# Kernel optimization log

Measured on AMD Instinct MI355X. Metric: run time of the kernel, lower is better.

## Reference

```python
import jax, jax.numpy as jnp
import numpy as np

B, N, C = 8, 4096, 512
H, DK, DV = 8, 64, 64


def _xnorm(x, gamma):
    # L2 norm over last dim, keepdim; scale by per-head gamma
    nrm = jnp.sqrt(jnp.sum(x * x, axis=-1, keepdims=True))
    return x * gamma / nrm


def setup_inputs() -> dict:
    key = jax.random.key(0)
    ks = jax.random.split(key, 9)
    inp = {
        "queries": jax.random.normal(ks[0], (B, N, C), dtype=jnp.float32),
        "keys": jax.random.normal(ks[1], (B, N, C), dtype=jnp.float32),
        "values": jax.random.normal(ks[2], (B, N, C), dtype=jnp.float32),
        # Linear weights stored torch-style [out, in]; init.normal_(std=0.001), bias=0
        "Wq": jax.random.normal(ks[3], (H * DK, C), dtype=jnp.float32) * 0.001,
        "bq": jnp.zeros((H * DK,), dtype=jnp.float32),
        "Wk": jax.random.normal(ks[4], (H * DK, C), dtype=jnp.float32) * 0.001,
        "bk": jnp.zeros((H * DK,), dtype=jnp.float32),
        "Wv": jax.random.normal(ks[5], (H * DV, C), dtype=jnp.float32) * 0.001,
        "bv": jnp.zeros((H * DV,), dtype=jnp.float32),
        "Wo": jax.random.normal(ks[6], (C, H * DV), dtype=jnp.float32) * 0.001,
        "bo": jnp.zeros((C,), dtype=jnp.float32),
        "gamma": jax.random.normal(ks[7], (1, H, 1, 1), dtype=jnp.float32),
    }
    return inp


def reference(queries, keys, values, Wq, bq, Wk, bk, Wv, bv, Wo, bo, gamma):
    bs, nq, _ = queries.shape
    nk = keys.shape[1]
    # projections -> [b, h, n, d]
    q = (queries @ Wq.T + bq).reshape(bs, nq, H, DK).transpose(0, 2, 1, 3)
    k = (keys @ Wk.T + bk).reshape(bs, nk, H, DK).transpose(0, 2, 1, 3)
    v = (values @ Wv.T + bv).reshape(bs, nk, H, DV).transpose(0, 2, 1, 3)
    # kv: [b, h, dk, dv]  (small intermediate)
    kv = jnp.einsum('bhnk,bhnv->bhkv', k, v)
    kv_n = _xnorm(kv, gamma)     # norm over dv
    q_n = _xnorm(q, gamma)       # norm over dk
    out = jnp.einsum('bhnk,bhkv->bhnv', q_n, kv_n)  # [b,h,nq,dv]
    out = out.transpose(0, 2, 1, 3).reshape(bs, nq, H * DV)
    return out @ Wo.T + bo
```

## Files before the change

kernel.cpp:

```cpp
#include <hip/hip_runtime.h>


typedef __attribute__((ext_vector_type(4))) float f32x4;
typedef __attribute__((ext_vector_type(8))) short s16x8;
typedef __attribute__((ext_vector_type(4))) unsigned short u16x4;
typedef __attribute__((ext_vector_type(8))) unsigned short u16x8;
typedef __attribute__((ext_vector_type(2))) unsigned u32x2;

#define DEVFN __device__ __forceinline__

DEVFN unsigned short f2b(float f) {
  union { float f; unsigned u; } un; un.f = f;
  unsigned r = un.u + 0x7fffu + ((un.u >> 16) & 1u);
  return (unsigned short)(r >> 16);
}
DEVFN float b2f(unsigned short us) {
  union { unsigned u; float f; } un; un.u = ((unsigned)us) << 16;
  return un.f;
}
DEVFN unsigned pk2(float x0, float x1) {
  union { float f; unsigned u; } a, b;
  a.f = x0; b.f = x1;
  return __builtin_amdgcn_perm(b.u + 0x8000u, a.u + 0x8000u, 0x07060302u);
}
DEVFN void gl_lds16(const void* g, void* l) {
  __builtin_amdgcn_global_load_lds(
      (const __attribute__((address_space(1))) unsigned*)g,
      (__attribute__((address_space(3))) unsigned*)l, 16, 0, 0);
}

template <bool AF32, typename CT>
DEVFN void gemmN512(const void* Ain, const unsigned short* Bt,
                    const float* bias, CT* C, bool qnorm,
                    const float* gamma, int bx) {
  __shared__ __align__(16) char LA[4][8192];
  __shared__ __align__(16) char LB[4][32768];
  const int tid = threadIdx.x, lane = tid & 63, wid = tid >> 6;
  const int r = lane & 15, g = lane >> 4;
  const int mw = wid >> 3;
  const int nw = wid & 7;

  const char* BsS = (const char*)Bt + (long)(wid * 32 + (lane >> 2)) * 1024 +
                    (((lane & 3) ^ ((lane >> 3) & 3)) * 16);

  const char* AfS = nullptr;
  const char* AsS = nullptr;
  int awr = 0;
  if constexpr (AF32) {
    AfS = (const char*)Ain + (long)(bx * 128 + (tid >> 3)) * 2048 +
          (tid & 7) * 16;
    const int row = tid >> 3, p = tid & 7;
    awr = row * 64 + (((p >> 1) ^ ((row >> 1) & 3)) << 4) + (p & 1) * 8;
  } else {
    AsS = (const char*)Ain + (long)(bx * 128 + wid * 16 + (lane >> 2)) * 1024 +
          (((lane & 3) ^ ((lane >> 3) & 3)) * 16);
  }

  f32x4 acc[4][4] = {};
  f32x4 paA, paB;

#define SGB(BUF, KT)                                                           \
  gl_lds16(BsS + (KT)*64, LB[BUF] + wid * 2048);                               \
  gl_lds16(BsS + 16384 + (KT)*64, LB[BUF] + wid * 2048 + 1024);
#define SGA(BUF, KT)                                                           \
  if (wid < 8) { gl_lds16(AsS + (KT)*64, LA[BUF] + wid * 1024); }
#define LDA(P, KT) P = *reinterpret_cast<const f32x4*>(AfS + (KT)*128);
#define WRA(P, BUF)                                                            \
  {                                                                            \
    u32x2 w;                                                                   \
    w[0] = pk2(P[0], P[1]);                                                    \
    w[1] = pk2(P[2], P[3]);                                                    \
    *reinterpret_cast<u32x2*>(LA[BUF] + awr) = w;                              \
  }
#define COMPUTE(BUF)                                                           \
  {                                                                            \
    s16x8 a[4], b[4];                                                          \
    _Pragma("unroll") for (int i = 0; i < 4; ++i) {                            \
      int ar = mw * 64 + i * 16 + r;                                           \
      a[i] = *reinterpret_cast<const s16x8*>(                                  \
          LA[BUF] + ar * 64 + ((g ^ ((ar >> 1) & 3)) << 4));                   \
    }                                                                          \
    _Pragma("unroll") for (int j = 0; j < 4; ++j) {                            \
      int br = nw * 64 + j * 16 + r;                                           \
      b[j] = *reinterpret_cast<const s16x8*>(                                  \
          LB[BUF] + br * 64 + ((g ^ ((br >> 1) & 3)) << 4));                   \
    }                                                                          \
    _Pragma("unroll") for (int i = 0; i < 4; ++i)                              \
        _Pragma("unroll") for (int j = 0; j < 4; ++j) acc[i][j] =              \
        __builtin_amdgcn_mfma_f32_16x16x32_bf16(a[i], b[j], acc[i][j], 0, 0,   \
                                                0);                            \
  }

  if constexpr (AF32) {
    LDA(paA, 0) WRA(paA, 0)
    LDA(paB, 1) WRA(paB, 1)
  } else {
    SGA(0, 0) SGA(1, 1)
  }
  SGB(0, 0) SGB(1, 1)
  __syncthreads();

#pragma unroll 1
  for (int t0 = 0; t0 < 14; t0 += 2) {
    const int b2 = (t0 + 2) & 3, b3 = (t0 + 3) & 3;
    if constexpr (AF32) {
      LDA(paA, t0 + 2) LDA(paB, t0 + 3)
    }
    SGB(b2, t0 + 2) SGB(b3, t0 + 3)
    if constexpr (!AF32) { SGA(b2, t0 + 2) SGA(b3, t0 + 3) }
    COMPUTE(t0 & 3)
    COMPUTE((t0 + 1) & 3)
    if constexpr (AF32) { WRA(paA, b2) WRA(paB, b3) }
    __syncthreads();
  }
  COMPUTE(2)
  COMPUTE(3)

#undef SGB
#undef SGA
#undef LDA
#undef WRA
#undef COMPUTE

  const int crow0 = bx * 128 + mw * 64 + g * 4;
  const int ccol0 = nw * 64 + r;
#pragma unroll
  for (int j = 0; j < 4; ++j) {
    float bv = bias[ccol0 + j * 16];
#pragma unroll
    for (int i = 0; i < 4; ++i)
#pragma unroll
      for (int ii = 0; ii < 4; ++ii) acc[i][j][ii] += bv;
  }
  if (qnorm) {
    const float gam = gamma[nw];
#pragma unroll
    for (int i = 0; i < 4; ++i)
#pragma unroll
      for (int ii = 0; ii < 4; ++ii) {
        float s = 0.f;
#pragma unroll
        for (int j = 0; j < 4; ++j) s += acc[i][j][ii] * acc[i][j][ii];
        s += __shfl_xor(s, 1);
        s += __shfl_xor(s, 2);
        s += __shfl_xor(s, 4);
        s += __shfl_xor(s, 8);
        float sc = gam / sqrtf(s);
#pragma unroll
        for (int j = 0; j < 4; ++j) acc[i][j][ii] *= sc;
      }
  }
#pragma unroll
  for (int i = 0; i < 4; ++i)
#pragma unroll
    for (int j = 0; j < 4; ++j)
#pragma unroll
      for (int ii = 0; ii < 4; ++ii) {
        long row = crow0 + i * 16 + ii;
        int col = ccol0 + j * 16;
        if constexpr (sizeof(CT) == 2)
          C[row * 512 + col] = f2b(acc[i][j][ii]);
        else
          C[row * 512 + col] = acc[i][j][ii];
      }
}

__global__ __launch_bounds__(1024, 4)
void proj_qkv(const float* __restrict__ Aq, const float* __restrict__ Ak,
              const float* __restrict__ Av, const unsigned short* __restrict__ Bq,
              const unsigned short* __restrict__ Bk, const unsigned short* __restrict__ Bv,
              const float* __restrict__ bq, const float* __restrict__ bk,
              const float* __restrict__ bv, unsigned short* __restrict__ Cq,
              unsigned short* __restrict__ Ck, unsigned short* __restrict__ Cv,
              const float* __restrict__ gamma) {
  const int z = blockIdx.y;
  const float* A = z == 0 ? Aq : (z == 1 ? Ak : Av);
  const unsigned short* B = z == 0 ? Bq : (z == 1 ? Bk : Bv);
  const float* bias = z == 0 ? bq : (z == 1 ? bk : bv);
  unsigned short* C = z == 0 ? Cq : (z == 1 ? Ck : Cv);
  gemmN512<true, unsigned short>(A, B, bias, C, z == 0, gamma, blockIdx.x);
}

__global__ __launch_bounds__(1024, 4)
void gemm_final(const unsigned short* __restrict__ q, const unsigned short* __restrict__ Mt,
                const float* __restrict__ bo, float* __restrict__ out) {
  const int zb = blockIdx.y;
  gemmN512<false, float>(q + (long)zb * 2097152, Mt + (long)zb * 262144, bo,
                         out + (long)zb * 2097152, false, nullptr, blockIdx.x);
}

#define NCHUNK 8
__global__ __launch_bounds__(256, 2)
void kv_partial(const unsigned short* __restrict__ kq,
                const unsigned short* __restrict__ vq,
                float* __restrict__ part) {
  const int tid = threadIdx.x;
  const int chunk = blockIdx.x;
  const int bh = blockIdx.y;
  const int b = bh >> 3, h = bh & 7;
  __shared__ float ks[32][64];
  __shared__ float vs[32][64];
  const int dk0 = (tid & 15) * 4;
  const int dv0 = (tid >> 4) * 4;
  float acc[4][4] = {};
  const long nbase = (long)b * 4096 + chunk * 512;
  const int lrow = tid >> 3, lc8 = tid & 7;

  for (int sub = 0; sub < 16; ++sub) {
    long n0 = nbase + sub * 32;
    {
      long gofs = (n0 + lrow) * 512 + h * 64 + lc8 * 8;
      u16x8 kk = *reinterpret_cast<const u16x8*>(kq + gofs);
      u16x8 vv = *reinterpret_cast<const u16x8*>(vq + gofs);
      f32x4 k0 = {b2f(kk[0]), b2f(kk[1]), b2f(kk[2]), b2f(kk[3])};
      f32x4 k1 = {b2f(kk[4]), b2f(kk[5]), b2f(kk[6]), b2f(kk[7])};
      f32x4 v0 = {b2f(vv[0]), b2f(vv[1]), b2f(vv[2]), b2f(vv[3])};
      f32x4 v1 = {b2f(vv[4]), b2f(vv[5]), b2f(vv[6]), b2f(vv[7])};
      *reinterpret_cast<f32x4*>(&ks[lrow][lc8 * 8]) = k0;
      *reinterpret_cast<f32x4*>(&ks[lrow][lc8 * 8 + 4]) = k1;
      *reinterpret_cast<f32x4*>(&vs[lrow][lc8 * 8]) = v0;
      *reinterpret_cast<f32x4*>(&vs[lrow][lc8 * 8 + 4]) = v1;
    }
    __syncthreads();
#pragma unroll 4
    for (int n = 0; n < 32; ++n) {
      f32x4 kk = *reinterpret_cast<const f32x4*>(&ks[n][dk0]);
      f32x4 vv = *reinterpret_cast<const f32x4*>(&vs[n][dv0]);
#pragma unroll
      for (int a = 0; a < 4; ++a)
#pragma unroll
        for (int c = 0; c < 4; ++c)
          acc[a][c] += kk[a] * vv[c];
    }
    __syncthreads();
  }
  float* pg = part + ((long)chunk * 64 + bh) * 4096;
#pragma unroll
  for (int a = 0; a < 4; ++a) {
    f32x4 o = {acc[a][0], acc[a][1], acc[a][2], acc[a][3]};
    *reinterpret_cast<f32x4*>(pg + (dk0 + a) * 64 + dv0) = o;
  }
}

__global__ __launch_bounds__(256)
void kv_norm_mt(const float* __restrict__ part, const float* __restrict__ gamma,
                const unsigned short* __restrict__ Wo_b,
                unsigned short* __restrict__ Mt) {
  const int bh = blockIdx.x, h = bh & 7, b = bh >> 3;
  const int tid = threadIdx.x;
  __shared__ float kvs[4096];
  __shared__ float scale_s[64];
  __shared__ __align__(16) unsigned short kvn_l[64 * 72];

#pragma unroll
  for (int i = 0; i < 4; ++i) {
    int e4 = i * 256 + tid;
    const float* p = part + (long)bh * 4096 + e4 * 4;
    f32x4 s = {0.f, 0.f, 0.f, 0.f};
#pragma unroll
    for (int c = 0; c < NCHUNK; ++c) {
      f32x4 v = *reinterpret_cast<const f32x4*>(p + (long)c * 64 * 4096);
      s += v;
    }
    *reinterpret_cast<f32x4*>(kvs + e4 * 4) = s;
  }
  __syncthreads();
  if (tid < 64) {
    float s = 0.f;
    for (int dv = 0; dv < 64; ++dv) { float x = kvs[tid * 64 + dv]; s += x * x; }
    scale_s[tid] = gamma[h] / sqrtf(s);
  }
  __syncthreads();
#pragma unroll
  for (int i = 0; i < 4; ++i) {
    int e4 = i * 256 + tid;
    int row = e4 >> 4, c0 = (e4 & 15) * 4;
    float sc = scale_s[row];
    f32x4 v = *reinterpret_cast<const f32x4*>(kvs + e4 * 4);
    u16x4 o = {f2b(v[0] * sc), f2b(v[1] * sc), f2b(v[2] * sc), f2b(v[3] * sc)};
    *reinterpret_cast<u16x4*>(kvn_l + row * 72 + c0) = o;
  }
  __syncthreads();

  const int seg = tid >> 6;
  const int lane = tid & 63;
  const int r = lane & 15, g = lane >> 4;
  f32x4 acc[8][4] = {};
  s16x8 bf[2][4];
#pragma unroll
  for (int ks = 0; ks < 2; ++ks)
#pragma unroll
    for (int j = 0; j < 4; ++j)
      bf[ks][j] = *reinterpret_cast<const s16x8*>(
          kvn_l + (j * 16 + r) * 72 + ks * 32 + g * 8);
#pragma unroll
  for (int ks = 0; ks < 2; ++ks)
#pragma unroll
    for (int i = 0; i < 8; ++i) {
      s16x8 af = *reinterpret_cast<const s16x8*>(
          Wo_b + (long)(seg * 128 + i * 16 + r) * 512 + h * 64 + ks * 32 + g * 8);
#pragma unroll
      for (int j = 0; j < 4; ++j)
        acc[i][j] = __builtin_amdgcn_mfma_f32_16x16x32_bf16(af, bf[ks][j], acc[i][j], 0, 0, 0);
    }
#pragma unroll
  for (int i = 0; i < 8; ++i)
#pragma unroll
    for (int j = 0; j < 4; ++j)
#pragma unroll
      for (int ii = 0; ii < 4; ++ii) {
        int c = seg * 128 + i * 16 + g * 4 + ii;
        int dk = j * 16 + r;
        Mt[(long)b * 262144 + (long)c * 512 + h * 64 + dk] = f2b(acc[i][j][ii]);
      }
}

__global__ void cast4(const float* __restrict__ a0, const float* __restrict__ a1,
                      const float* __restrict__ a2, const float* __restrict__ a3,
                      unsigned short* __restrict__ o0, unsigned short* __restrict__ o1,
                      unsigned short* __restrict__ o2, unsigned short* __restrict__ o3) {
  const int y = blockIdx.y;
  const float* in = y == 0 ? a0 : (y == 1 ? a1 : (y == 2 ? a2 : a3));
  unsigned short* out = y == 0 ? o0 : (y == 1 ? o1 : (y == 2 ? o2 : o3));
  int i = blockIdx.x * 256 + threadIdx.x;
  f32x4 v = reinterpret_cast<const f32x4*>(in)[i];
  reinterpret_cast<u16x4*>(out)[i] = u16x4{f2b(v[0]), f2b(v[1]), f2b(v[2]), f2b(v[3])};
}

extern "C" void kernel_launch(void* const* d_in, const int* in_sizes, int n_in,
                              void* d_out, int out_size, void* d_ws, size_t ws_size,
                              hipStream_t stream) {
  const float* queries = (const float*)d_in[0];
  const float* keys    = (const float*)d_in[1];
  const float* values  = (const float*)d_in[2];
  const float* Wq = (const float*)d_in[3];
  const float* bq = (const float*)d_in[4];
  const float* Wk = (const float*)d_in[5];
  const float* bk = (const float*)d_in[6];
  const float* Wv = (const float*)d_in[7];
  const float* bv = (const float*)d_in[8];
  const float* Wo = (const float*)d_in[9];
  const float* bo = (const float*)d_in[10];
  const float* gamma = (const float*)d_in[11];

  unsigned short* Wq_b = (unsigned short*)d_ws;
  unsigned short* Wk_b = Wq_b + 262144;
  unsigned short* Wv_b = Wk_b + 262144;
  unsigned short* Wo_b = Wv_b + 262144;
  unsigned short* q_b  = Wo_b + 262144;
  unsigned short* kvn  = q_b + 16777216;
  float* part = (float*)(kvn + 262144);
  unsigned short* Mt = (unsigned short*)(part + 2097152);
  unsigned short* k_b = (unsigned short*)d_out;
  unsigned short* v_b = k_b + 16777216;
  float* out = (float*)d_out;

  cast4<<<dim3(256, 4), 256, 0, stream>>>(Wq, Wk, Wv, Wo, Wq_b, Wk_b, Wv_b, Wo_b);

  proj_qkv<<<dim3(256, 3), 1024, 0, stream>>>(
      queries, keys, values, Wq_b, Wk_b, Wv_b, bq, bk, bv, q_b, k_b, v_b, gamma);

  kv_partial<<<dim3(NCHUNK, 64), 256, 0, stream>>>(k_b, v_b, part);
  kv_norm_mt<<<64, 256, 0, stream>>>(part, gamma, Wo_b, Mt);

  gemm_final<<<dim3(32, 8), 1024, 0, stream>>>(q_b, Mt, bo, out);
}
```

Before: 167.4 us.

## Restructure kv_partial so each wave owns a full 64x64 tile over row slices

The kv_partial kernel no longer stages K and V tiles through shared memory with per-subtile barriers. Each wave now reads bf16 K/V rows straight from global memory into registers and accumulates a full 64x64 outer-product tile over its own 128-row slice, with each lane holding an 8x8 block. The four wave partials are then reduced serially through shared memory before a coalesced store. This removes LDS traffic and barriers from the inner loop, but raises register pressure to 64 accumulators per lane, relies on global loads without LDS reuse, and adds a serialized cross-wave reduction.

```diff
diff --git a/kernel.cpp b/kernel.cpp
--- a/kernel.cpp
+++ b/kernel.cpp
@@ -194,51 +194,63 @@
 void kv_partial(const unsigned short* __restrict__ kq,
                 const unsigned short* __restrict__ vq,
                 float* __restrict__ part) {
-  const int tid = threadIdx.x;
+  const int tid = threadIdx.x, lane = tid & 63, wid = tid >> 6;
   const int chunk = blockIdx.x;
   const int bh = blockIdx.y;
   const int b = bh >> 3, h = bh & 7;
-  __shared__ float ks[32][64];
-  __shared__ float vs[32][64];
-  const int dk0 = (tid & 15) * 4;
-  const int dv0 = (tid >> 4) * 4;
-  float acc[4][4] = {};
-  const long nbase = (long)b * 4096 + chunk * 512;
-  const int lrow = tid >> 3, lc8 = tid & 7;
-
-  for (int sub = 0; sub < 16; ++sub) {
-    long n0 = nbase + sub * 32;
-    {
-      long gofs = (n0 + lrow) * 512 + h * 64 + lc8 * 8;
-      u16x8 kk = *reinterpret_cast<const u16x8*>(kq + gofs);
-      u16x8 vv = *reinterpret_cast<const u16x8*>(vq + gofs);
-      f32x4 k0 = {b2f(kk[0]), b2f(kk[1]), b2f(kk[2]), b2f(kk[3])};
-      f32x4 k1 = {b2f(kk[4]), b2f(kk[5]), b2f(kk[6]), b2f(kk[7])};
-      f32x4 v0 = {b2f(vv[0]), b2f(vv[1]), b2f(vv[2]), b2f(vv[3])};
-      f32x4 v1 = {b2f(vv[4]), b2f(vv[5]), b2f(vv[6]), b2f(vv[7])};
-      *reinterpret_cast<f32x4*>(&ks[lrow][lc8 * 8]) = k0;
-      *reinterpret_cast<f32x4*>(&ks[lrow][lc8 * 8 + 4]) = k1;
-      *reinterpret_cast<f32x4*>(&vs[lrow][lc8 * 8]) = v0;
-      *reinterpret_cast<f32x4*>(&vs[lrow][lc8 * 8 + 4]) = v1;
+  const int dk0 = (lane & 7) * 8;
+  const int dv0 = (lane >> 3) * 8;
+  __shared__ float red[4096];
+
+  f32x4 acc[8][2] = {};
+  const long nbase = (long)b * 4096 + chunk * 512 + wid * 128;
+  const unsigned short* kp = kq + nbase * 512 + h * 64 + dk0;
+  const unsigned short* vp = vq + nbase * 512 + h * 64 + dv0;
+
+#pragma unroll 4
+  for (int n = 0; n < 128; ++n) {
+    u16x8 kk = *reinterpret_cast<const u16x8*>(kp + (long)n * 512);
+    u16x8 vv = *reinterpret_cast<const u16x8*>(vp + (long)n * 512);
+    float kf[8];
+#pragma unroll
+    for (int i = 0; i < 8; ++i) kf[i] = b2f(kk[i]);
+    f32x4 v0 = {b2f(vv[0]), b2f(vv[1]), b2f(vv[2]), b2f(vv[3])};
+    f32x4 v1 = {b2f(vv[4]), b2f(vv[5]), b2f(vv[6]), b2f(vv[7])};
+#pragma unroll
+    for (int a = 0; a < 8; ++a) {
+      acc[a][0] += v0 * kf[a];
+      acc[a][1] += v1 * kf[a];
+    }
+  }
+
+  if (wid == 0) {
+#pragma unroll
+    for (int a = 0; a < 8; ++a) {
+      *reinterpret_cast<f32x4*>(&red[(dk0 + a) * 64 + dv0]) = acc[a][0];
+      *reinterpret_cast<f32x4*>(&red[(dk0 + a) * 64 + dv0 + 4]) = acc[a][1];
+    }
+  }
+  __syncthreads();
+#pragma unroll 1
+  for (int w = 1; w < 4; ++w) {
+    if (wid == w) {
+#pragma unroll
+      for (int a = 0; a < 8; ++a) {
+        f32x4* p0 = reinterpret_cast<f32x4*>(&red[(dk0 + a) * 64 + dv0]);
+        f32x4* p1 = reinterpret_cast<f32x4*>(&red[(dk0 + a) * 64 + dv0 + 4]);
+        *p0 += acc[a][0];
+        *p1 += acc[a][1];
+      }
     }
     __syncthreads();
-#pragma unroll 4
-    for (int n = 0; n < 32; ++n) {
-      f32x4 kk = *reinterpret_cast<const f32x4*>(&ks[n][dk0]);
-      f32x4 vv = *reinterpret_cast<const f32x4*>(&vs[n][dv0]);
-#pragma unroll
-      for (int a = 0; a < 4; ++a)
-#pragma unroll
-        for (int c = 0; c < 4; ++c)
-          acc[a][c] += kk[a] * vv[c];
-    }
-    __syncthreads();
-  }
+  }
+
   float* pg = part + ((long)chunk * 64 + bh) * 4096;
 #pragma unroll
-  for (int a = 0; a < 4; ++a) {
-    f32x4 o = {acc[a][0], acc[a][1], acc[a][2], acc[a][3]};
-    *reinterpret_cast<f32x4*>(pg + (dk0 + a) * 64 + dv0) = o;
+  for (int i = 0; i < 4; ++i) {
+    int e4 = i * 256 + tid;
+    *reinterpret_cast<f32x4*>(pg + e4 * 4) =
+        *reinterpret_cast<const f32x4*>(red + e4 * 4);
   }
 }
 
```

New measurement: 166.9 us. No clear change (-0.3%).
